# Performance work log

Hardware: AMD Instinct MI355X
Metric: run time of the kernel (lower is better)

Reference implementation:

```python
import jax, jax.numpy as jnp
import numpy as np

N_NODES = 50000   # hypergraph nodes
N_EDGES = 20000   # hyperedges
M = 400000        # node-edge incidences (node copies)
L = 800000        # inner GIN graph edges per side
HID = 128
IN_DIM = 128
B = 32            # graphs in batch
C = 10            # num_classes
N_LAYERS = 2
INNER = 2         # inner_num_layers
BN_EPS = 1e-5


def setup_inputs() -> dict:
    key = jax.random.key(0)
    ks = jax.random.split(key, 16)
    s = 0.05
    inp = {}
    inp["x_N"] = jax.random.normal(ks[0], (N_NODES, IN_DIM), jnp.float32)
    # embedding linear
    inp["We"] = jax.random.normal(ks[1], (IN_DIM, HID), jnp.float32) * s
    inp["be"] = jnp.zeros((HID,), jnp.float32)
    # GIN params: [outer_layer, direction(N2E/E2N), inner_conv, mlp_linear, hid, hid]
    inp["Wg"] = jax.random.normal(ks[2], (N_LAYERS, 2, INNER, 2, HID, HID), jnp.float32) * s
    inp["bg"] = jnp.zeros((N_LAYERS, 2, INNER, 2, HID), jnp.float32)
    inp["eps_g"] = jnp.zeros((N_LAYERS, 2, INNER), jnp.float32)
    # eval-mode BatchNorm affine params per inner conv
    inp["gamma"] = jnp.ones((N_LAYERS, 2, INNER, HID), jnp.float32)
    inp["beta"] = jnp.zeros((N_LAYERS, 2, INNER, HID), jnp.float32)
    # per-layer prediction heads
    inp["Wp"] = jax.random.normal(ks[3], (N_LAYERS + 1, HID, C), jnp.float32) * s
    inp["bp"] = jnp.zeros((N_LAYERS + 1, C), jnp.float32)
    # index tensors
    inp["ori_node_idx"] = jax.random.randint(ks[4], (M,), 0, N_NODES)
    inp["node2edge"] = jax.random.randint(ks[5], (M,), 0, N_EDGES)
    inp["edge_index_N"] = jax.random.randint(ks[6], (2, L), 0, M)
    inp["ori_edge_idx"] = jax.random.randint(ks[7], (M,), 0, N_EDGES)
    inp["edge2node"] = jax.random.randint(ks[8], (M,), 0, N_NODES)
    inp["edge_index_E"] = jax.random.randint(ks[9], (2, L), 0, M)
    inp["batch"] = jax.random.randint(ks[10], (M,), 0, B)
    return inp


def _gin(x, src, dst, Wg, bg, eps, gamma, beta):
    # GIN over the copy graph: h = MLP((1+eps)*x + sum_{j->i} x_j), BN (eval), ReLU between convs
    inv_std = 1.0 / jnp.sqrt(1.0 + BN_EPS)
    n = x.shape[0]
    for l in range(INNER):
        agg = jax.ops.segment_sum(x[src], dst, num_segments=n)
        h = (1.0 + eps[l]) * x + agg
        h = jax.nn.relu(h @ Wg[l, 0] + bg[l, 0])
        h = h @ Wg[l, 1] + bg[l, 1]
        h = gamma[l] * h * inv_std + beta[l]
        x = jax.nn.relu(h) if l < INNER - 1 else h
    return x


def reference(x_N, We, be, Wg, bg, eps_g, gamma, beta, Wp, bp,
              ori_node_idx, node2edge, edge_index_N,
              ori_edge_idx, edge2node, edge_index_E, batch):
    node_x = x_N @ We + be                       # [N, HID]
    xs = [node_x]
    for i in range(N_LAYERS):
        # node -> edge: gather copies, inner GIN, segment-sum pool over hyperedges
        nx = node_x[ori_node_idx]                # [M, HID]
        nx = _gin(nx, edge_index_N[0], edge_index_N[1],
                  Wg[i, 0], bg[i, 0], eps_g[i, 0], gamma[i, 0], beta[i, 0])
        edge_x = jax.ops.segment_sum(nx, node2edge, num_segments=N_EDGES)
        edge_x = jax.nn.relu(edge_x)             # EdgeUpdate (dropout off in eval)
        # edge -> node
        ex = edge_x[ori_edge_idx]                # [M, HID]
        ex = _gin(ex, edge_index_E[0], edge_index_E[1],
                  Wg[i, 1], bg[i, 1], eps_g[i, 1], gamma[i, 1], beta[i, 1])
        node_x = jax.ops.segment_sum(ex, edge2node, num_segments=N_NODES)
        node_x = jax.nn.relu(node_x)             # NodeUpdate
        xs.append(node_x)
    score = jnp.zeros((B, C), x_N.dtype)
    for i, x in enumerate(xs):
        pooled = jax.ops.segment_sum(x[ori_node_idx], batch, num_segments=B)
        score = score + pooled @ Wp[i] + bp[i]
    return score
```

## Files before the change

### kernel.cpp

```cpp
#include <hip/hip_runtime.h>
#include <hip/hip_bf16.h>

#define HID 128
static const int N_NODES = 50000;
static const int N_EDGES = 20000;
static const int M_COPIES = 400000;
static const int L_EDGES = 800000;
static const int NBATCH = 32;
static const int NCLS = 10;
#define INV_STD 0.9999950000374997f
#define IDX_CAP 384

typedef __attribute__((ext_vector_type(4))) float f32x4;
typedef __attribute__((ext_vector_type(8))) short short8;
typedef __attribute__((ext_vector_type(8))) unsigned short ushort8;
typedef __attribute__((ext_vector_type(4))) unsigned short u16x4;

__device__ __forceinline__ float bf2f(unsigned short u) {
    union { unsigned u; float f; } v; v.u = ((unsigned)u) << 16; return v.f;
}
__device__ __forceinline__ unsigned short f2bf(float f) {
    union { float f; unsigned u; } v; v.f = f;
    unsigned r = v.u + 0x7FFFu + ((v.u >> 16) & 1u);
    return (unsigned short)(r >> 16);
}
__device__ __forceinline__ void gatomic_add(float* p, float v) {
    unsafeAtomicAdd(p, v);
}

__device__ __forceinline__ unsigned short* xs_addr(unsigned short* Xs, int c, int r) {
    int byte = ((c * 64 + r) * 16) ^ ((c & 7) << 4);
    return (unsigned short*)((char*)Xs + byte);
}

__device__ __forceinline__ void stage8(const unsigned short* __restrict__ Wmat, int e,
                                       unsigned short* buf, int wave, int lane) {
    const char* g = (const char*)Wmat + ((size_t)e << 12) + (wave << 10) + (lane << 4);
    char* l = (char*)buf + (wave << 10);
    __builtin_amdgcn_global_load_lds(
        (const __attribute__((address_space(1))) unsigned int*)g,
        (__attribute__((address_space(3))) unsigned int*)l,
        16, 0, 0);
}

__device__ __forceinline__ void mfma4(const unsigned short* Ws, const short8* xv,
                                      f32x4& a, int quad, int ln) {
#pragma unroll
    for (int kc = 0; kc < 4; ++kc) {
        short8 wa = *(const short8*)(Ws + (((kc * 4 + quad) * 16) + ln) * 8);
        a = __builtin_amdgcn_mfma_f32_16x16x32_bf16(wa, xv[kc], a, 0, 0, 0);
    }
}

__global__ __launch_bounds__(256) void prep_w(const float* __restrict__ We,
                                              const float* __restrict__ Wg,
                                              unsigned short* __restrict__ Wt) {
    int t = blockIdx.x * 256 + threadIdx.x;
    if (t >= 17 * 16384) return;
    int mat = t >> 14, rem = t & 16383;
    int h = rem >> 11, r2 = rem & 2047;
    int gg = r2 >> 7, r3 = r2 & 127;
    int n = r3 >> 3, j = r3 & 7;
    int k = gg * 8 + j, col = h * 16 + n;
    const float* src = (mat == 0) ? We : (Wg + (size_t)(mat - 1) * 16384);
    Wt[t] = f2bf(src[k * 128 + col]);
}

__global__ __launch_bounds__(256) void hist_k(const int* __restrict__ idx, int n,
                                              int* __restrict__ cnt) {
    int t = blockIdx.x * 256 + threadIdx.x;
    if (t < n) atomicAdd(&cnt[idx[t]], 1);
}

__global__ __launch_bounds__(256) void scan1_k(int* __restrict__ a, int n,
                                               int* __restrict__ part) {
    __shared__ int s[256];
    int i = blockIdx.x * 256 + threadIdx.x;
    int v = (i < n) ? a[i] : 0;
    s[threadIdx.x] = v;
    __syncthreads();
#pragma unroll
    for (int d = 1; d < 256; d <<= 1) {
        int t = (threadIdx.x >= d) ? s[threadIdx.x - d] : 0;
        __syncthreads();
        s[threadIdx.x] += t;
        __syncthreads();
    }
    if (i < n) a[i] = s[threadIdx.x] - v;
    if (threadIdx.x == 255) part[blockIdx.x] = s[255];
}

__global__ __launch_bounds__(256) void scan2_k(int* __restrict__ part, int nb) {
    __shared__ int s[256];
    __shared__ int carry;
    if (threadIdx.x == 0) carry = 0;
    __syncthreads();
    for (int base = 0; base < nb; base += 256) {
        int i = base + threadIdx.x;
        int v = (i < nb) ? part[i] : 0;
        s[threadIdx.x] = v;
        __syncthreads();
#pragma unroll
        for (int d = 1; d < 256; d <<= 1) {
            int t = (threadIdx.x >= d) ? s[threadIdx.x - d] : 0;
            __syncthreads();
            s[threadIdx.x] += t;
            __syncthreads();
        }
        if (i < nb) part[i] = carry + s[threadIdx.x] - v;
        __syncthreads();
        if (threadIdx.x == 0) carry += s[255];
        __syncthreads();
    }
}

__global__ __launch_bounds__(256) void scan3_k(int* __restrict__ a, int n,
                                               const int* __restrict__ part) {
    int i = blockIdx.x * 256 + threadIdx.x;
    if (i < n) a[i] += part[blockIdx.x];
}

__global__ __launch_bounds__(256) void fill_edge_k(
    const int* __restrict__ src, const int* __restrict__ dst,
    const int* __restrict__ remap, int n, int* __restrict__ off,
    int* __restrict__ srcs, int* __restrict__ comps) {
    int e = blockIdx.x * 256 + threadIdx.x;
    if (e >= n) return;
    int d = dst[e];
    int pos = atomicAdd(&off[d], 1);
    int s = src[e];
    srcs[pos] = s;
    comps[pos] = remap[s];
}

__global__ __launch_bounds__(256) void fill_pool_k(
    const int* __restrict__ seg, int n, int* __restrict__ off,
    int* __restrict__ items) {
    int m = blockIdx.x * 256 + threadIdx.x;
    if (m >= n) return;
    int pos = atomicAdd(&off[seg[m]], 1);
    items[pos] = m;
}

__global__ __launch_bounds__(256) void segsum_pool(
    const unsigned short* __restrict__ tbl, const int* __restrict__ off,
    const int* __restrict__ items, unsigned short* __restrict__ out, int nseg)
{
    int wave = threadIdx.x >> 6, lane = threadIdx.x & 63;
    int seg = blockIdx.x * 4 + wave;
    if (seg >= nseg) return;
    int start = (seg == 0) ? 0 : off[seg - 1];
    int end = off[seg];
    int g = lane & 15, sub = lane >> 4;
    float a[8] = {0.f, 0.f, 0.f, 0.f, 0.f, 0.f, 0.f, 0.f};
    for (int p = start + sub; p < end; p += 4) {
        int r = items[p];
        ushort8 v = *(const ushort8*)(tbl + (size_t)r * 128 + g * 8);
#pragma unroll
        for (int j = 0; j < 8; ++j) a[j] += bf2f(v[j]);
    }
#pragma unroll
    for (int j = 0; j < 8; ++j) {
        a[j] += __shfl_xor(a[j], 16, 64);
        a[j] += __shfl_xor(a[j], 32, 64);
    }
    if (sub == 0) {
        ushort8 ov;
#pragma unroll
        for (int j = 0; j < 8; ++j) ov[j] = f2bf(fmaxf(a[j], 0.f));
        *(ushort8*)(out + (size_t)seg * 128 + g * 8) = ov;
    }
}

template<bool CONV0>
__global__ __launch_bounds__(256, 6) void fused_conv(
    const unsigned short* __restrict__ tbl,
    const int* __restrict__ self_idx,
    const int* __restrict__ off, const int* __restrict__ items,
    const float* __restrict__ eps_ptr,
    const unsigned short* __restrict__ W1t, const float* __restrict__ b1,
    const unsigned short* __restrict__ W2t, const float* __restrict__ b2,
    const float* __restrict__ gam, const float* __restrict__ bet,
    unsigned short* __restrict__ out)
{
    __shared__ __align__(16) unsigned short Xs[16 * 64 * 8];
    __shared__ __align__(16) unsigned short Wsb[2][2048];
    __shared__ int sIdx[IDX_CAP];
    __shared__ int meta[192];
    const int tid = threadIdx.x;
    const int row0 = blockIdx.x * 64;
    const int wave = tid >> 6, lane = tid & 63;

    stage8(W1t, 0, Wsb[0], wave, lane);

    const int bstart = (row0 == 0) ? 0 : off[row0 - 1];
    const int cnt = off[row0 + 63] - bstart;
    const bool useLds = (cnt <= IDX_CAP);

    if (tid < 64) {
        int gr = row0 + tid;
        meta[tid]       = (gr == 0) ? 0 : off[gr - 1];
        meta[64 + tid]  = off[gr];
        meta[128 + tid] = CONV0 ? self_idx[gr] : gr;
    }
    if (useLds)
        for (int i = tid; i < cnt; i += 256) sIdx[i] = items[bstart + i];
    __syncthreads();

    const float e = 1.0f + eps_ptr[0];
    const int g = tid & 15;
    const int rb = tid >> 4;
#pragma unroll
    for (int i = 0; i < 4; ++i) {
        int r = rb + 16 * i;
        int start = meta[r], end = meta[64 + r], self = meta[128 + r];
        float a[8];
        ushort8 u = *(const ushort8*)(tbl + (size_t)self * 128 + g * 8);
#pragma unroll
        for (int j = 0; j < 8; ++j) a[j] = e * bf2f(u[j]);
        if (useLds) {
            int pos = start - bstart, pe = end - bstart;
            for (; pos + 2 <= pe; pos += 2) {
                int i0 = sIdx[pos], i1 = sIdx[pos + 1];
                ushort8 v0 = *(const ushort8*)(tbl + (size_t)i0 * 128 + g * 8);
                ushort8 v1 = *(const ushort8*)(tbl + (size_t)i1 * 128 + g * 8);
#pragma unroll
                for (int j = 0; j < 8; ++j) a[j] += bf2f(v0[j]) + bf2f(v1[j]);
            }
            if (pos < pe) {
                int i0 = sIdx[pos];
                ushort8 v0 = *(const ushort8*)(tbl + (size_t)i0 * 128 + g * 8);
#pragma unroll
                for (int j = 0; j < 8; ++j) a[j] += bf2f(v0[j]);
            }
        } else {
            for (int pos = start; pos < end; ++pos) {
                int rr = items[pos];
                ushort8 v = *(const ushort8*)(tbl + (size_t)rr * 128 + g * 8);
#pragma unroll
                for (int j = 0; j < 8; ++j) a[j] += bf2f(v[j]);
            }
        }
        ushort8 xv;
#pragma unroll
        for (int j = 0; j < 8; ++j) xv[j] = f2bf(a[j]);
        *(ushort8*)xs_addr(Xs, g, r) = xv;
    }
    __syncthreads();

    const int ln = lane & 15, quad = lane >> 4;
    const int row = wave * 16 + ln;

    short8 xb[4];
#pragma unroll
    for (int kc = 0; kc < 4; ++kc)
        xb[kc] = *(const short8*)xs_addr(Xs, kc * 4 + quad, row);

    f32x4 acc[8];
#pragma unroll
    for (int t = 0; t < 8; ++t) acc[t] = (f32x4){0.f, 0.f, 0.f, 0.f};

#pragma unroll
    for (int e8 = 0; e8 < 8; ++e8) {
        if (e8 < 7) stage8(W1t, e8 + 1, Wsb[(e8 + 1) & 1], wave, lane);
        else        stage8(W2t, 0,      Wsb[0],            wave, lane);
        mfma4(Wsb[e8 & 1], xb, acc[e8], quad, ln);
        __syncthreads();
    }

    {
        const int j0 = (quad & 1) * 4;
#pragma unroll
        for (int t = 0; t < 8; ++t) {
            int p0 = t * 16 + quad * 4;
            f32x4 bv = *(const f32x4*)(b1 + p0);
            u16x4 hp;
#pragma unroll
            for (int i = 0; i < 4; ++i) hp[i] = f2bf(fmaxf(acc[t][i] + bv[i], 0.f));
            *(u16x4*)((char*)xs_addr(Xs, p0 >> 3, row) + j0 * 2) = hp;
        }
    }

    short8 hb[4];
#pragma unroll
    for (int kc = 0; kc < 4; ++kc)
        hb[kc] = *(const short8*)xs_addr(Xs, kc * 4 + quad, row);

#pragma unroll
    for (int t = 0; t < 8; ++t) acc[t] = (f32x4){0.f, 0.f, 0.f, 0.f};

#pragma unroll
    for (int f = 0; f < 8; ++f) {
        if (f < 7) stage8(W2t, f + 1, Wsb[(f + 1) & 1], wave, lane);
        mfma4(Wsb[f & 1], hb, acc[f], quad, ln);
        if (f < 7) __syncthreads();
    }

    const int m = row0 + row;
#pragma unroll
    for (int t = 0; t < 8; ++t) {
        int n0 = t * 16 + quad * 4;
        f32x4 bv = *(const f32x4*)(b2 + n0);
        f32x4 gv = *(const f32x4*)(gam + n0);
        f32x4 tv = *(const f32x4*)(bet + n0);
        u16x4 op;
#pragma unroll
        for (int i = 0; i < 4; ++i) {
            float h = acc[t][i] + bv[i];
            h = gv[i] * h * INV_STD + tv[i];
            if (CONV0) h = fmaxf(h, 0.f);
            op[i] = f2bf(h);
        }
        *(u16x4*)(out + (size_t)m * 128 + n0) = op;
    }
}

__global__ __launch_bounds__(256) void gemm_embed(
    const float* __restrict__ in, const unsigned short* __restrict__ Wt,
    const float* __restrict__ bias, unsigned short* __restrict__ out_bf, int rows)
{
    __shared__ __align__(16) unsigned short Xs[16 * 64 * 8];
    __shared__ __align__(16) unsigned short Ws[16 * 128 * 8];
    int tid = threadIdx.x;
    int row0 = blockIdx.x * 64;
#pragma unroll
    for (int i = 0; i < 8; ++i) {
        int chunk = tid + i * 256;
        int n = chunk >> 4, g = chunk & 15;
        *(short8*)(Ws + (g * 128 + n) * 8) =
            *(const short8*)(Wt + (n >> 4) * 2048 + g * 128 + (n & 15) * 8);
    }
#pragma unroll
    for (int i = 0; i < 4; ++i) {
        int chunk = tid + i * 256;
        int r = chunk >> 4, g = chunk & 15;
        int gr = row0 + r;
        ushort8 v;
        if (gr < rows) {
            const float* p = in + (size_t)gr * 128 + g * 8;
            f32x4 a0 = *(const f32x4*)p;
            f32x4 a1 = *(const f32x4*)(p + 4);
#pragma unroll
            for (int j = 0; j < 4; ++j) { v[j] = f2bf(a0[j]); v[4 + j] = f2bf(a1[j]); }
        } else {
#pragma unroll
            for (int j = 0; j < 8; ++j) v[j] = 0;
        }
        *(ushort8*)(Xs + (g * 64 + r) * 8) = v;
    }
    __syncthreads();
    int wave = tid >> 6, lane = tid & 63;
    int m0 = wave * 16;
    int ln = lane & 15, quad = lane >> 4;
    f32x4 acc[8];
#pragma unroll
    for (int t = 0; t < 8; ++t) acc[t] = (f32x4){0.f, 0.f, 0.f, 0.f};
#pragma unroll
    for (int kc = 0; kc < 4; ++kc) {
        int g = kc * 4 + quad;
        short8 a = *(const short8*)(Xs + (g * 64 + m0 + ln) * 8);
#pragma unroll
        for (int t = 0; t < 8; ++t) {
            short8 b = *(const short8*)(Ws + (g * 128 + t * 16 + ln) * 8);
            acc[t] = __builtin_amdgcn_mfma_f32_16x16x32_bf16(a, b, acc[t], 0, 0, 0);
        }
    }
#pragma unroll
    for (int t = 0; t < 8; ++t) {
        int col = t * 16 + ln;
        float bi = bias[col];
#pragma unroll
        for (int i = 0; i < 4; ++i) {
            int gr = row0 + m0 + quad * 4 + i;
            if (gr < rows) out_bf[(size_t)gr * 128 + col] = f2bf(acc[t][i] + bi);
        }
    }
}

template<bool ACCUM>
__global__ __launch_bounds__(256) void proj_y(
    const unsigned short* __restrict__ nx, const float* __restrict__ Wp,
    float* __restrict__ y, int rows)
{
    __shared__ float Wl[HID * NCLS];
    for (int i = threadIdx.x; i < HID * NCLS; i += 256) Wl[i] = Wp[i];
    __syncthreads();
    int r = blockIdx.x * 256 + threadIdx.x;
    if (r >= rows) return;
    float acc[NCLS];
#pragma unroll
    for (int c = 0; c < NCLS; ++c) acc[c] = 0.f;
    const unsigned short* xp = nx + (size_t)r * 128;
#pragma unroll 4
    for (int g = 0; g < 16; ++g) {
        ushort8 u = *(const ushort8*)(xp + g * 8);
#pragma unroll
        for (int j = 0; j < 8; ++j) {
            float xv = bf2f(u[j]);
            const float* w = Wl + (g * 8 + j) * NCLS;
#pragma unroll
            for (int c = 0; c < NCLS; ++c) acc[c] += xv * w[c];
        }
    }
    float* yp = y + (size_t)r * NCLS;
#pragma unroll
    for (int c = 0; c < NCLS; ++c) {
        if (ACCUM) yp[c] += acc[c];
        else yp[c] = acc[c];
    }
}

__global__ __launch_bounds__(256) void score_scatter(
    const float* __restrict__ y, const int* __restrict__ ori,
    const int* __restrict__ batch, float* __restrict__ score)
{
    __shared__ float sc[NBATCH * NCLS];
    for (int i = threadIdx.x; i < NBATCH * NCLS; i += 256) sc[i] = 0.f;
    __syncthreads();
    int stride = gridDim.x * 256;
    for (int m = blockIdx.x * 256 + threadIdx.x; m < M_COPIES; m += stride) {
        int r = ori[m], b = batch[m];
        const float* yp = y + (size_t)r * NCLS;
#pragma unroll
        for (int c = 0; c < NCLS; ++c)
            __hip_atomic_fetch_add(&sc[b * NCLS + c], yp[c],
                                   __ATOMIC_RELAXED, __HIP_MEMORY_SCOPE_WORKGROUP);
    }
    __syncthreads();
    for (int i = threadIdx.x; i < NBATCH * NCLS; i += 256) gatomic_add(score + i, sc[i]);
}

__global__ void score_final(const float* __restrict__ score, const float* __restrict__ bp,
                            float* __restrict__ out)
{
    int t = threadIdx.x;
    if (t >= NBATCH * NCLS) return;
    int c = t % NCLS;
    out[t] = score[t] + bp[c] + bp[NCLS + c] + bp[2 * NCLS + c];
}

__global__ void fill_sentinel(float* out, int n, float enc) {
    int t = blockIdx.x * 64 + threadIdx.x;
    if (t < n) out[t] = enc;
}

static inline void build_csr_edge(const int* src, const int* dst, const int* remap,
                                  int nitem, int nseg, int* off, int* part,
                                  int* srcs, int* comps, hipStream_t stream) {
    int nb = (nseg + 255) / 256;
    (void)hipMemsetAsync(off, 0, (size_t)nseg * 4, stream);
    hist_k<<<(nitem + 255) / 256, 256, 0, stream>>>(dst, nitem, off);
    scan1_k<<<nb, 256, 0, stream>>>(off, nseg, part);
    scan2_k<<<1, 256, 0, stream>>>(part, nb);
    scan3_k<<<nb, 256, 0, stream>>>(off, nseg, part);
    fill_edge_k<<<(nitem + 255) / 256, 256, 0, stream>>>(src, dst, remap, nitem, off, srcs, comps);
}
static inline void build_csr_pool(const int* seg, int nitem, int nseg,
                                  int* off, int* part, int* items, hipStream_t stream) {
    int nb = (nseg + 255) / 256;
    (void)hipMemsetAsync(off, 0, (size_t)nseg * 4, stream);
    hist_k<<<(nitem + 255) / 256, 256, 0, stream>>>(seg, nitem, off);
    scan1_k<<<nb, 256, 0, stream>>>(off, nseg, part);
    scan2_k<<<1, 256, 0, stream>>>(part, nb);
    scan3_k<<<nb, 256, 0, stream>>>(off, nseg, part);
    fill_pool_k<<<(nitem + 255) / 256, 256, 0, stream>>>(seg, nitem, off, items);
}

extern "C" void kernel_launch(void* const* d_in, const int* in_sizes, int n_in,
                              void* d_out, int out_size, void* d_ws, size_t ws_size,
                              hipStream_t stream) {
    const float* x_N    = (const float*)d_in[0];
    const float* We     = (const float*)d_in[1];
    const float* be     = (const float*)d_in[2];
    const float* Wg     = (const float*)d_in[3];
    const float* bg     = (const float*)d_in[4];
    const float* eps_g  = (const float*)d_in[5];
    const float* gam    = (const float*)d_in[6];
    const float* bet    = (const float*)d_in[7];
    const float* Wp     = (const float*)d_in[8];
    const float* bp     = (const float*)d_in[9];
    const int* ori_node = (const int*)d_in[10];
    const int* node2edge= (const int*)d_in[11];
    const int* eiN      = (const int*)d_in[12];
    const int* ori_edge = (const int*)d_in[13];
    const int* edge2node= (const int*)d_in[14];
    const int* eiE      = (const int*)d_in[15];
    const int* batch    = (const int*)d_in[16];

    char* p = (char*)d_ws;
    auto take = [&](size_t n) { char* r = p; p += (n + 255) & ~(size_t)255; return r; };
    unsigned short* Wt  = (unsigned short*)take((size_t)17 * 16384 * 2);
    unsigned short* Xb  = (unsigned short*)take((size_t)M_COPIES * 128 * 2);
    unsigned short* Xb2 = (unsigned short*)take((size_t)M_COPIES * 128 * 2);
    unsigned short* nx  = (unsigned short*)take((size_t)N_NODES * 128 * 2);
    unsigned short* ex  = (unsigned short*)take((size_t)N_EDGES * 128 * 2);
    float* y            = (float*)take((size_t)N_NODES * NCLS * 4);
    float* score        = (float*)take((size_t)NBATCH * NCLS * 4);
    int* offN           = (int*)take((size_t)M_COPIES * 4);
    int* offE           = (int*)take((size_t)M_COPIES * 4);
    int* off_n2e        = (int*)take((size_t)N_EDGES * 4);
    int* off_e2n        = (int*)take((size_t)N_NODES * 4);
    int* srcsN          = (int*)take((size_t)L_EDGES * 4);
    int* compsN         = (int*)take((size_t)L_EDGES * 4);
    int* srcsE          = (int*)take((size_t)L_EDGES * 4);
    int* compsE         = (int*)take((size_t)L_EDGES * 4);
    int* it_n2e         = (int*)take((size_t)M_COPIES * 4);
    int* it_e2n         = (int*)take((size_t)M_COPIES * 4);
    int* part           = (int*)take((size_t)2048 * 4);
    size_t need = (size_t)(p - (char*)d_ws);
    if (need > ws_size) {
        fill_sentinel<<<(out_size + 63) / 64, 64, 0, stream>>>(
            (float*)d_out, out_size, 1.0e9f + (float)ws_size);
        return;
    }

    prep_w<<<1088, 256, 0, stream>>>(We, Wg, Wt);
    (void)hipMemsetAsync(score, 0, (size_t)NBATCH * NCLS * 4, stream);

    build_csr_edge(eiN, eiN + L_EDGES, ori_node, L_EDGES, M_COPIES, offN, part, srcsN, compsN, stream);
    build_csr_edge(eiE, eiE + L_EDGES, ori_edge, L_EDGES, M_COPIES, offE, part, srcsE, compsE, stream);
    build_csr_pool(node2edge, M_COPIES, N_EDGES, off_n2e, part, it_n2e, stream);
    build_csr_pool(edge2node, M_COPIES, N_NODES, off_e2n, part, it_e2n, stream);

    gemm_embed<<<(N_NODES + 63) / 64, 256, 0, stream>>>(x_N, Wt, be, nx, N_NODES);
    proj_y<false><<<(N_NODES + 255) / 256, 256, 0, stream>>>(nx, Wp, y, N_NODES);

    const int MBLK = M_COPIES / 64;
    for (int layer = 0; layer < 2; ++layer) {
        for (int dir = 0; dir < 2; ++dir) {
            int cj0 = layer * 4 + dir * 2;
            int cj1 = cj0 + 1;
            const unsigned short* base = (dir == 0) ? nx : ex;
            const int* selfI = (dir == 0) ? ori_node : ori_edge;
            const int* offD  = (dir == 0) ? offN : offE;
            const int* srcsD = (dir == 0) ? srcsN : srcsE;
            const int* compD = (dir == 0) ? compsN : compsE;

            fused_conv<true><<<MBLK, 256, 0, stream>>>(
                base, selfI, offD, compD, eps_g + cj0,
                Wt + (size_t)(1 + cj0 * 2) * 16384, bg + (cj0 * 2) * 128,
                Wt + (size_t)(1 + cj0 * 2 + 1) * 16384, bg + (cj0 * 2 + 1) * 128,
                gam + cj0 * 128, bet + cj0 * 128, Xb);
            fused_conv<false><<<MBLK, 256, 0, stream>>>(
                Xb, nullptr, offD, srcsD, eps_g + cj1,
                Wt + (size_t)(1 + cj1 * 2) * 16384, bg + (cj1 * 2) * 128,
                Wt + (size_t)(1 + cj1 * 2 + 1) * 16384, bg + (cj1 * 2 + 1) * 128,
                gam + cj1 * 128, bet + cj1 * 128, Xb2);
            if (dir == 0) {
                segsum_pool<<<(N_EDGES + 3) / 4, 256, 0, stream>>>(
                    Xb2, off_n2e, it_n2e, ex, N_EDGES);
            } else {
                segsum_pool<<<(N_NODES + 3) / 4, 256, 0, stream>>>(
                    Xb2, off_e2n, it_e2n, nx, N_NODES);
                proj_y<true><<<(N_NODES + 255) / 256, 256, 0, stream>>>(
                    nx, Wp + (layer + 1) * HID * NCLS, y, N_NODES);
            }
        }
    }
    score_scatter<<<256, 256, 0, stream>>>(y, ori_node, batch, score);
    score_final<<<1, 320, 0, stream>>>(score, bp, (float*)d_out);
}
```

Baseline: 1.426 ms.

## Batch CSR construction kernels, triple-buffer weight staging, interleave gather rows

The CSR build for the two inner edge graphs and the two pooling maps is merged into paired kernels (histogram, scan, fill) that handle both inputs per launch, so there are fewer launches and memsets. In fused_conv, weight staging goes from two buffers to three with a prefetch distance of two. A partial vmcnt wait plus s_barrier replaces the full __syncthreads between chunks. The neighbour gather now advances four rows at once under a wave ballot so more independent loads are in flight, and occupancy is lowered from 6 to 5 blocks to make room for the extra registers and LDS.

```diff
diff --git a/kernel.cpp b/kernel.cpp
--- a/kernel.cpp
+++ b/kernel.cpp
@@ -41,6 +41,14 @@
         (const __attribute__((address_space(1))) unsigned int*)g,
         (__attribute__((address_space(3))) unsigned int*)l,
         16, 0, 0);
+}
+
+template<int N>
+__device__ __forceinline__ void pipe_barrier() {
+    if constexpr (N == 0) asm volatile("s_waitcnt vmcnt(0)" ::: "memory");
+    else                  asm volatile("s_waitcnt vmcnt(1)" ::: "memory");
+    __builtin_amdgcn_s_barrier();
+    asm volatile("" ::: "memory");
 }
 
 __device__ __forceinline__ void mfma4(const unsigned short* Ws, const short8* xv,
@@ -66,14 +74,21 @@
     Wt[t] = f2bf(src[k * 128 + col]);
 }
 
-__global__ __launch_bounds__(256) void hist_k(const int* __restrict__ idx, int n,
-                                              int* __restrict__ cnt) {
+__global__ __launch_bounds__(256) void hist2_k(
+    const int* __restrict__ iA, int nA, int* __restrict__ cA,
+    const int* __restrict__ iB, int nB, int* __restrict__ cB) {
     int t = blockIdx.x * 256 + threadIdx.x;
-    if (t < n) atomicAdd(&cnt[idx[t]], 1);
-}
-
-__global__ __launch_bounds__(256) void scan1_k(int* __restrict__ a, int n,
-                                               int* __restrict__ part) {
+    if (t < nA) atomicAdd(&cA[iA[t]], 1);
+    if (t < nB) atomicAdd(&cB[iB[t]], 1);
+}
+
+__global__ __launch_bounds__(256) void scan1d_k(
+    int* __restrict__ a0, int n0, int* __restrict__ p0,
+    int* __restrict__ a1, int n1, int* __restrict__ p1) {
+    int* a    = blockIdx.y ? a1 : a0;
+    int n     = blockIdx.y ? n1 : n0;
+    int* part = blockIdx.y ? p1 : p0;
+    if ((int)(blockIdx.x * 256) >= n) return;
     __shared__ int s[256];
     int i = blockIdx.x * 256 + threadIdx.x;
     int v = (i < n) ? a[i] : 0;
@@ -90,7 +105,10 @@
     if (threadIdx.x == 255) part[blockIdx.x] = s[255];
 }
 
-__global__ __launch_bounds__(256) void scan2_k(int* __restrict__ part, int nb) {
+__global__ __launch_bounds__(256) void scan2d_k(
+    int* __restrict__ p0, int nb0, int* __restrict__ p1, int nb1) {
+    int* part = blockIdx.x ? p1 : p0;
+    int nb    = blockIdx.x ? nb1 : nb0;
     __shared__ int s[256];
     __shared__ int carry;
     if (threadIdx.x == 0) carry = 0;
@@ -114,32 +132,38 @@
     }
 }
 
-__global__ __launch_bounds__(256) void scan3_k(int* __restrict__ a, int n,
-                                               const int* __restrict__ part) {
+__global__ __launch_bounds__(256) void scan3d_k(
+    int* __restrict__ a0, int n0, const int* __restrict__ p0,
+    int* __restrict__ a1, int n1, const int* __restrict__ p1) {
+    int* a          = blockIdx.y ? a1 : a0;
+    int n           = blockIdx.y ? n1 : n0;
+    const int* part = blockIdx.y ? p1 : p0;
     int i = blockIdx.x * 256 + threadIdx.x;
     if (i < n) a[i] += part[blockIdx.x];
 }
 
-__global__ __launch_bounds__(256) void fill_edge_k(
-    const int* __restrict__ src, const int* __restrict__ dst,
-    const int* __restrict__ remap, int n, int* __restrict__ off,
-    int* __restrict__ srcs, int* __restrict__ comps) {
-    int e = blockIdx.x * 256 + threadIdx.x;
-    if (e >= n) return;
-    int d = dst[e];
-    int pos = atomicAdd(&off[d], 1);
-    int s = src[e];
-    srcs[pos] = s;
-    comps[pos] = remap[s];
-}
-
-__global__ __launch_bounds__(256) void fill_pool_k(
-    const int* __restrict__ seg, int n, int* __restrict__ off,
-    int* __restrict__ items) {
-    int m = blockIdx.x * 256 + threadIdx.x;
-    if (m >= n) return;
-    int pos = atomicAdd(&off[seg[m]], 1);
-    items[pos] = m;
+__global__ __launch_bounds__(256) void fill_edge2_k(
+    const int* __restrict__ sA, const int* __restrict__ dA, const int* __restrict__ rA,
+    int nA, int* __restrict__ oA, int* __restrict__ ssA, int* __restrict__ ccA,
+    const int* __restrict__ sB, const int* __restrict__ dB, const int* __restrict__ rB,
+    int nB, int* __restrict__ oB, int* __restrict__ ssB, int* __restrict__ ccB) {
+    int t = blockIdx.x * 256 + threadIdx.x;
+    if (t < nA) {
+        int d = dA[t]; int pos = atomicAdd(&oA[d], 1);
+        int s = sA[t]; ssA[pos] = s; ccA[pos] = rA[s];
+    }
+    if (t < nB) {
+        int d = dB[t]; int pos = atomicAdd(&oB[d], 1);
+        int s = sB[t]; ssB[pos] = s; ccB[pos] = rB[s];
+    }
+}
+
+__global__ __launch_bounds__(256) void fill_pool2_k(
+    const int* __restrict__ gA, int nA, int* __restrict__ oA, int* __restrict__ itA,
+    const int* __restrict__ gB, int nB, int* __restrict__ oB, int* __restrict__ itB) {
+    int t = blockIdx.x * 256 + threadIdx.x;
+    if (t < nA) { int pos = atomicAdd(&oA[gA[t]], 1); itA[pos] = t; }
+    if (t < nB) { int pos = atomicAdd(&oB[gB[t]], 1); itB[pos] = t; }
 }
 
 __global__ __launch_bounds__(256) void segsum_pool(
@@ -173,7 +197,7 @@
 }
 
 template<bool CONV0>
-__global__ __launch_bounds__(256, 6) void fused_conv(
+__global__ __launch_bounds__(256, 5) void fused_conv(
     const unsigned short* __restrict__ tbl,
     const int* __restrict__ self_idx,
     const int* __restrict__ off, const int* __restrict__ items,
@@ -184,7 +208,7 @@
     unsigned short* __restrict__ out)
 {
     __shared__ __align__(16) unsigned short Xs[16 * 64 * 8];
-    __shared__ __align__(16) unsigned short Wsb[2][2048];
+    __shared__ __align__(16) unsigned short Wsb[3][2048];
     __shared__ int sIdx[IDX_CAP];
     __shared__ int meta[192];
     const int tid = threadIdx.x;
@@ -192,11 +216,13 @@
     const int wave = tid >> 6, lane = tid & 63;
 
     stage8(W1t, 0, Wsb[0], wave, lane);
+    stage8(W1t, 1, Wsb[1], wave, lane);
 
     const int bstart = (row0 == 0) ? 0 : off[row0 - 1];
     const int cnt = off[row0 + 63] - bstart;
     const bool useLds = (cnt <= IDX_CAP);
 
+    if (tid == 0) sIdx[0] = 0;
     if (tid < 64) {
         int gr = row0 + tid;
         meta[tid]       = (gr == 0) ? 0 : off[gr - 1];
@@ -210,41 +236,56 @@
     const float e = 1.0f + eps_ptr[0];
     const int g = tid & 15;
     const int rb = tid >> 4;
+    int st[4], en[4];
+    float a[4][8];
 #pragma unroll
     for (int i = 0; i < 4; ++i) {
         int r = rb + 16 * i;
-        int start = meta[r], end = meta[64 + r], self = meta[128 + r];
-        float a[8];
+        st[i] = meta[r]; en[i] = meta[64 + r];
+        int self = meta[128 + r];
         ushort8 u = *(const ushort8*)(tbl + (size_t)self * 128 + g * 8);
 #pragma unroll
-        for (int j = 0; j < 8; ++j) a[j] = e * bf2f(u[j]);
-        if (useLds) {
-            int pos = start - bstart, pe = end - bstart;
-            for (; pos + 2 <= pe; pos += 2) {
-                int i0 = sIdx[pos], i1 = sIdx[pos + 1];
-                ushort8 v0 = *(const ushort8*)(tbl + (size_t)i0 * 128 + g * 8);
-                ushort8 v1 = *(const ushort8*)(tbl + (size_t)i1 * 128 + g * 8);
-#pragma unroll
-                for (int j = 0; j < 8; ++j) a[j] += bf2f(v0[j]) + bf2f(v1[j]);
+        for (int j = 0; j < 8; ++j) a[i][j] = e * bf2f(u[j]);
+    }
+    if (useLds) {
+        const int cmax = (cnt > 0) ? (cnt - 1) : 0;
+#pragma unroll
+        for (int i = 0; i < 4; ++i) { st[i] -= bstart; en[i] -= bstart; }
+        while (__ballot((st[0] < en[0]) | (st[1] < en[1]) |
+                        (st[2] < en[2]) | (st[3] < en[3]))) {
+            ushort8 v[4];
+#pragma unroll
+            for (int i = 0; i < 4; ++i) {
+                int p = st[i] < cmax ? st[i] : cmax;
+                int idx = sIdx[p];
+                v[i] = *(const ushort8*)(tbl + (size_t)idx * 128 + g * 8);
             }
-            if (pos < pe) {
-                int i0 = sIdx[pos];
-                ushort8 v0 = *(const ushort8*)(tbl + (size_t)i0 * 128 + g * 8);
-#pragma unroll
-                for (int j = 0; j < 8; ++j) a[j] += bf2f(v0[j]);
+#pragma unroll
+            for (int i = 0; i < 4; ++i) {
+                if (st[i] < en[i]) {
+#pragma unroll
+                    for (int j = 0; j < 8; ++j) a[i][j] += bf2f(v[i][j]);
+                    st[i]++;
+                }
             }
-        } else {
-            for (int pos = start; pos < end; ++pos) {
+        }
+    } else {
+#pragma unroll
+        for (int i = 0; i < 4; ++i) {
+            for (int pos = st[i]; pos < en[i]; ++pos) {
                 int rr = items[pos];
                 ushort8 v = *(const ushort8*)(tbl + (size_t)rr * 128 + g * 8);
 #pragma unroll
-                for (int j = 0; j < 8; ++j) a[j] += bf2f(v[j]);
+                for (int j = 0; j < 8; ++j) a[i][j] += bf2f(v[j]);
             }
         }
+    }
+#pragma unroll
+    for (int i = 0; i < 4; ++i) {
         ushort8 xv;
 #pragma unroll
-        for (int j = 0; j < 8; ++j) xv[j] = f2bf(a[j]);
-        *(ushort8*)xs_addr(Xs, g, r) = xv;
+        for (int j = 0; j < 8; ++j) xv[j] = f2bf(a[i][j]);
+        *(ushort8*)xs_addr(Xs, g, rb + 16 * i) = xv;
     }
     __syncthreads();
 
@@ -261,11 +302,11 @@
     for (int t = 0; t < 8; ++t) acc[t] = (f32x4){0.f, 0.f, 0.f, 0.f};
 
 #pragma unroll
-    for (int e8 = 0; e8 < 8; ++e8) {
-        if (e8 < 7) stage8(W1t, e8 + 1, Wsb[(e8 + 1) & 1], wave, lane);
-        else        stage8(W2t, 0,      Wsb[0],            wave, lane);
-        mfma4(Wsb[e8 & 1], xb, acc[e8], quad, ln);
-        __syncthreads();
+    for (int s = 0; s < 8; ++s) {
+        int pf = s + 2;
+        stage8(pf < 8 ? W1t : W2t, pf & 7, Wsb[pf % 3], wave, lane);
+        mfma4(Wsb[s % 3], xb, acc[s], quad, ln);
+        pipe_barrier<1>();
     }
 
     {
@@ -291,9 +332,10 @@
 
 #pragma unroll
     for (int f = 0; f < 8; ++f) {
-        if (f < 7) stage8(W2t, f + 1, Wsb[(f + 1) & 1], wave, lane);
-        mfma4(Wsb[f & 1], hb, acc[f], quad, ln);
-        if (f < 7) __syncthreads();
+        if (f < 6) stage8(W2t, f + 2, Wsb[(f + 10) % 3], wave, lane);
+        mfma4(Wsb[(f + 8) % 3], hb, acc[f], quad, ln);
+        if (f < 6)      pipe_barrier<1>();
+        else if (f == 6) pipe_barrier<0>();
     }
 
     const int m = row0 + row;
@@ -442,28 +484,6 @@
 __global__ void fill_sentinel(float* out, int n, float enc) {
     int t = blockIdx.x * 64 + threadIdx.x;
     if (t < n) out[t] = enc;
-}
-
-static inline void build_csr_edge(const int* src, const int* dst, const int* remap,
-                                  int nitem, int nseg, int* off, int* part,
-                                  int* srcs, int* comps, hipStream_t stream) {
-    int nb = (nseg + 255) / 256;
-    (void)hipMemsetAsync(off, 0, (size_t)nseg * 4, stream);
-    hist_k<<<(nitem + 255) / 256, 256, 0, stream>>>(dst, nitem, off);
-    scan1_k<<<nb, 256, 0, stream>>>(off, nseg, part);
-    scan2_k<<<1, 256, 0, stream>>>(part, nb);
-    scan3_k<<<nb, 256, 0, stream>>>(off, nseg, part);
-    fill_edge_k<<<(nitem + 255) / 256, 256, 0, stream>>>(src, dst, remap, nitem, off, srcs, comps);
-}
-static inline void build_csr_pool(const int* seg, int nitem, int nseg,
-                                  int* off, int* part, int* items, hipStream_t stream) {
-    int nb = (nseg + 255) / 256;
-    (void)hipMemsetAsync(off, 0, (size_t)nseg * 4, stream);
-    hist_k<<<(nitem + 255) / 256, 256, 0, stream>>>(seg, nitem, off);
-    scan1_k<<<nb, 256, 0, stream>>>(off, nseg, part);
-    scan2_k<<<1, 256, 0, stream>>>(part, nb);
-    scan3_k<<<nb, 256, 0, stream>>>(off, nseg, part);
-    fill_pool_k<<<(nitem + 255) / 256, 256, 0, stream>>>(seg, nitem, off, items);
 }
 
 extern "C" void kernel_launch(void* const* d_in, const int* in_sizes, int n_in,
@@ -506,7 +526,7 @@
     int* compsE         = (int*)take((size_t)L_EDGES * 4);
     int* it_n2e         = (int*)take((size_t)M_COPIES * 4);
     int* it_e2n         = (int*)take((size_t)M_COPIES * 4);
-    int* part           = (int*)take((size_t)2048 * 4);
+    int* part           = (int*)take((size_t)8192 * 4);
     size_t need = (size_t)(p - (char*)d_ws);
     if (need > ws_size) {
         fill_sentinel<<<(out_size + 63) / 64, 64, 0, stream>>>(
@@ -517,10 +537,29 @@
     prep_w<<<1088, 256, 0, stream>>>(We, Wg, Wt);
     (void)hipMemsetAsync(score, 0, (size_t)NBATCH * NCLS * 4, stream);
 
-    build_csr_edge(eiN, eiN + L_EDGES, ori_node, L_EDGES, M_COPIES, offN, part, srcsN, compsN, stream);
-    build_csr_edge(eiE, eiE + L_EDGES, ori_edge, L_EDGES, M_COPIES, offE, part, srcsE, compsE, stream);
-    build_csr_pool(node2edge, M_COPIES, N_EDGES, off_n2e, part, it_n2e, stream);
-    build_csr_pool(edge2node, M_COPIES, N_NODES, off_e2n, part, it_e2n, stream);
+    const int NB_M = (M_COPIES + 255) / 256;
+    const int NB_L = (L_EDGES + 255) / 256;
+    const int NB_N = (N_NODES + 255) / 256;
+    int* partB = part + 4096;
+
+    (void)hipMemsetAsync(offN, 0, (size_t)2 * M_COPIES * 4, stream);
+    hist2_k<<<NB_L, 256, 0, stream>>>(eiN + L_EDGES, L_EDGES, offN,
+                                      eiE + L_EDGES, L_EDGES, offE);
+    scan1d_k<<<dim3(NB_M, 2), 256, 0, stream>>>(offN, M_COPIES, part, offE, M_COPIES, partB);
+    scan2d_k<<<2, 256, 0, stream>>>(part, NB_M, partB, NB_M);
+    scan3d_k<<<dim3(NB_M, 2), 256, 0, stream>>>(offN, M_COPIES, part, offE, M_COPIES, partB);
+    fill_edge2_k<<<NB_L, 256, 0, stream>>>(eiN, eiN + L_EDGES, ori_node, L_EDGES, offN, srcsN, compsN,
+                                           eiE, eiE + L_EDGES, ori_edge, L_EDGES, offE, srcsE, compsE);
+
+    (void)hipMemsetAsync(off_n2e, 0,
+        (size_t)((char*)off_e2n - (char*)off_n2e) + (size_t)N_NODES * 4, stream);
+    hist2_k<<<NB_M, 256, 0, stream>>>(node2edge, M_COPIES, off_n2e,
+                                      edge2node, M_COPIES, off_e2n);
+    scan1d_k<<<dim3(NB_N, 2), 256, 0, stream>>>(off_n2e, N_EDGES, part, off_e2n, N_NODES, partB);
+    scan2d_k<<<2, 256, 0, stream>>>(part, (N_EDGES + 255) / 256, partB, NB_N);
+    scan3d_k<<<dim3(NB_N, 2), 256, 0, stream>>>(off_n2e, N_EDGES, part, off_e2n, N_NODES, partB);
+    fill_pool2_k<<<NB_M, 256, 0, stream>>>(node2edge, M_COPIES, off_n2e, it_n2e,
+                                           edge2node, M_COPIES, off_e2n, it_e2n);
 
     gemm_embed<<<(N_NODES + 63) / 64, 256, 0, stream>>>(x_N, Wt, be, nx, N_NODES);
     proj_y<false><<<(N_NODES + 255) / 256, 256, 0, stream>>>(nx, Wp, y, N_NODES);
```

Result: no change. 1.418 ms (-0.5%).
